# Performance work log

Hardware: AMD Instinct MI355X
Metric: run time of the kernel (lower is better)

The kernel has to match this reference:

```python
import jax, jax.numpy as jnp
import numpy as np

B, H, D = 2048, 50, 400          # batch, history_length, news/category embed dim
S, C = 285, 18                   # num_subcategories, num_categories
NC = 50                          # num_clicks_embed_dim (= history_length table size)
FILL = 1e-30                     # masked_fill value used by the original module


def setup_inputs() -> dict:
    key = jax.random.key(0)
    ks = jax.random.split(key, 9)
    vectors = jax.random.normal(ks[0], (B, H, D), dtype=jnp.float32)
    subcategory = jax.random.randint(ks[1], (B, H), 0, S, dtype=jnp.int32)
    category = jax.random.randint(ks[2], (B, H), 0, C, dtype=jnp.int32)
    subcat_embed = jax.random.normal(ks[3], (S, D), dtype=jnp.float32) * 0.02
    cat_embed = jax.random.normal(ks[4], (C, D), dtype=jnp.float32) * 0.02
    clicks_embed = jax.random.normal(ks[5], (H, NC), dtype=jnp.float32) * 0.02
    w_news = jax.random.normal(ks[6], (D,), dtype=jnp.float32) * 0.05
    w_subcat = jax.random.normal(ks[7], (D + NC,), dtype=jnp.float32) * 0.05
    w_cat = jax.random.normal(ks[8], (D + NC,), dtype=jnp.float32) * 0.05
    return {"vectors": vectors, "subcategory": subcategory, "category": category,
            "subcat_embed": subcat_embed, "cat_embed": cat_embed,
            "clicks_embed": clicks_embed, "w_news": w_news,
            "w_subcat": w_subcat, "w_cat": w_cat}


def reference(vectors, subcategory, category, subcat_embed, cat_embed,
              clicks_embed, w_news, w_subcat, w_cat):
    sub_mask = jax.nn.one_hot(subcategory, S, dtype=vectors.dtype)   # [B,H,S]
    cat_mask = jax.nn.one_hot(category, C, dtype=vectors.dtype)      # [B,H,C]
    sub_to_cat = jnp.einsum('bhs,bhc->bsc', sub_mask, cat_mask)      # [B,S,C]

    # --- news -> subcategory attention pooling ---
    news_scores = jnp.einsum('bhd,d->bh', vectors, w_news)           # [B,H]
    scores = jnp.where(sub_mask > 0, news_scores[:, :, None], FILL)  # [B,H,S]
    news_w = jax.nn.softmax(scores, axis=1)
    sub_news_repr = jnp.einsum('bhs,bhd->bsd', news_w, vectors)      # [B,S,D]
    sub_repr = sub_news_repr + subcat_embed[None]                    # [B,S,D]

    sub_clicks = sub_mask.sum(axis=1)                                # [B,S] float counts
    sub_weights = sub_clicks / sub_clicks.sum(axis=1, keepdims=True)
    sub_clicks_emb = clicks_embed[sub_clicks.astype(jnp.int32)]      # [B,S,NC]

    # --- subcategory -> category attention pooling ---
    sc_scores = jnp.einsum('bsk,k->bs',
                           jnp.concatenate([sub_repr, sub_clicks_emb], axis=2),
                           w_subcat)                                 # [B,S]
    scores2 = jnp.where(sub_to_cat > 0, sc_scores[:, :, None], FILL) # [B,S,C]
    sub_w = jax.nn.softmax(scores2, axis=1)
    cat_sub_repr = jnp.einsum('bsc,bsd->bcd', sub_w, sub_repr)       # [B,C,D]
    cat_repr = cat_sub_repr + cat_embed[None]                        # [B,C,D]

    cat_clicks = cat_mask.sum(axis=1)                                # [B,C]
    cat_weights = cat_clicks / cat_clicks.sum(axis=1, keepdims=True)
    cat_clicks_emb = clicks_embed[cat_clicks.astype(jnp.int32)]      # [B,C,NC]

    # --- category -> user attention pooling (unmasked) ---
    c_scores = jnp.einsum('bck,k->bc',
                          jnp.concatenate([cat_repr, cat_clicks_emb], axis=2),
                          w_cat)                                     # [B,C]
    cat_w = jax.nn.softmax(c_scores, axis=1)
    user_repr = jnp.einsum('bc,bcd->bd', cat_w, cat_repr)            # [B,D]

    return (sub_repr, sub_weights, cat_repr, cat_weights, user_repr)
```

## Files before the change

### kernel.cpp

```cpp
#include <hip/hip_runtime.h>

#define BB 2048
#define HH 50
#define DD 400
#define D4 100
#define SS 285
#define CC 18
#define NCC 50
#define FILLV 1e-30f

static constexpr int BLOCK = 256;

static constexpr size_t OFF1 = (size_t)BB * SS * DD;
static constexpr size_t OFF2 = OFF1 + (size_t)BB * SS;
static constexpr size_t OFF3 = OFF2 + (size_t)BB * CC * DD;
static constexpr size_t OFF4 = OFF3 + (size_t)BB * CC;

#define WS_ETOT 0
#define WS_SCE  400
#define WS_SEW  688
#define WS_CEDS 976
#define WS_CEDC 1026
#define WS_CEW  1076

typedef float f4 __attribute__((ext_vector_type(4)));

__device__ __forceinline__ float dot4(f4 a, f4 b) {
    return a.x * b.x + a.y * b.y + a.z * b.z + a.w * b.w;
}

__global__ void hierec_pre(const float* __restrict__ subcat_embed,
                           const float* __restrict__ cat_embed,
                           const float* __restrict__ clicks_embed,
                           const float* __restrict__ w_subcat,
                           const float* __restrict__ w_cat,
                           float* __restrict__ ws)
{
    const int tid  = threadIdx.x;
    const int lane = tid & 63;
    const int wave = tid >> 6;
    const int wpb  = blockDim.x >> 6;
    const int gw   = blockIdx.x * wpb + wave;
    const int nw   = gridDim.x * wpb;

    for (int s = gw; s < SS; s += nw) {
        float p1 = 0.f, p2 = 0.f;
        for (int d = lane; d < DD; d += 64) {
            float v = subcat_embed[s * DD + d];
            p1 += v * w_subcat[d];
            p2 += v * w_cat[d];
        }
        for (int off = 32; off; off >>= 1) {
            p1 += __shfl_down(p1, off);
            p2 += __shfl_down(p2, off);
        }
        if (lane == 0) { ws[WS_SCE + s] = p1; ws[WS_SEW + s] = p2; }
    }
    if (blockIdx.x == 0) {
        for (int d = tid; d < DD; d += blockDim.x) {
            float a = 0.f;
            for (int s = 0; s < SS; ++s) a += subcat_embed[s * DD + d];
            ws[WS_ETOT + d] = a;
        }
    }
    if (blockIdx.x == 1) {
        for (int k = wave; k < HH; k += wpb) {
            float p1 = 0.f, p2 = 0.f;
            if (lane < NCC) {
                float v = clicks_embed[k * NCC + lane];
                p1 = v * w_subcat[DD + lane];
                p2 = v * w_cat[DD + lane];
            }
            for (int off = 32; off; off >>= 1) {
                p1 += __shfl_down(p1, off);
                p2 += __shfl_down(p2, off);
            }
            if (lane == 0) { ws[WS_CEDS + k] = p1; ws[WS_CEDC + k] = p2; }
        }
    }
    if (blockIdx.x == 2) {
        for (int c = wave; c < CC; c += wpb) {
            float p = 0.f;
            for (int d = lane; d < DD; d += 64) p += cat_embed[c * DD + d] * w_cat[d];
            for (int off = 32; off; off >>= 1) p += __shfl_down(p, off);
            if (lane == 0) ws[WS_CEW + c] = p;
        }
    }
}

__global__ __launch_bounds__(BLOCK, 8) void hierec_main(
    const float* __restrict__ vectors,
    const int*   __restrict__ subcategory,
    const int*   __restrict__ category,
    const float* __restrict__ subcat_embed,
    const float* __restrict__ cat_embed,
    const float* __restrict__ w_news,
    const float* __restrict__ w_subcat,
    const float* __restrict__ w_cat,
    const float* __restrict__ pre,
    float* __restrict__ out)
{
    const int b    = blockIdx.x;
    const int tid  = threadIdx.x;
    const int lane = tid & 63;
    const int wave = tid >> 6;

    __shared__ f4     vt4L[D4];
    __shared__ f4     et4L[D4];
    __shared__ float  coefS[SS];
    __shared__ unsigned long long maskS[SS];
    __shared__ int    cntS[SS];
    __shared__ float  ns1L[HH], ns2L[HH], ns3L[HH];
    __shared__ float  uzL[HH], wNL[HH], scL[HH];
    __shared__ unsigned long long maskL[HH];
    __shared__ int    hsL[HH], hcL[HH], repL[HH], prepL[HH];
    __shared__ float  GmL[CC][HH];
    __shared__ float  mcL[CC], ucL[CC], rZcL[CC], AL[CC], csL[CC], catwL[CC];
    __shared__ int    cntcL[CC];
    __shared__ int    prepCL[HH], prepSL[HH];
    __shared__ float  prepGL[HH];
    __shared__ int    clickedL[HH];
    __shared__ int    unclkL[SS];
    __shared__ int    npL, ndL, nUcnt;
    __shared__ float  PvL, vtwL, etwL;

    const float* vb  = vectors + (size_t)b * HH * DD;
    const f4*    vb4 = (const f4*)vb;
    const f4*    se4 = (const f4*)subcat_embed;
    const f4*    ce4 = (const f4*)cat_embed;

    if (tid < HH) {
        hsL[tid] = subcategory[b * HH + tid];
        hcL[tid] = category[b * HH + tid];
    }
    for (int s = tid; s < SS; s += BLOCK) {
        coefS[s] = 1.f / (float)HH;
        maskS[s] = 0ull;
        cntS[s]  = 0;
    }
    if (tid < D4) {
        et4L[tid] = ((const f4*)pre)[tid];
        f4 z = {0.f, 0.f, 0.f, 0.f};
        vt4L[tid] = z;
    }
    if (tid == 0) nUcnt = 0;
    __syncthreads();

    {
        const f4* wn4 = (const f4*)w_news;
        const f4* ws4 = (const f4*)w_subcat;
        const f4* wc4 = (const f4*)w_cat;
        const bool hi = lane < (D4 - 64);
        f4 vtp0 = {0.f, 0.f, 0.f, 0.f};
        f4 vtp1 = {0.f, 0.f, 0.f, 0.f};
        for (int h = wave; h < HH; h += 4) {
            f4 v0 = __builtin_nontemporal_load(&vb4[h * D4 + lane]);
            float p1 = dot4(v0, wn4[lane]);
            float p2 = dot4(v0, ws4[lane]);
            float p3 = dot4(v0, wc4[lane]);
            vtp0 += v0;
            if (hi) {
                f4 v1 = __builtin_nontemporal_load(&vb4[h * D4 + 64 + lane]);
                p1 += dot4(v1, wn4[64 + lane]);
                p2 += dot4(v1, ws4[64 + lane]);
                p3 += dot4(v1, wc4[64 + lane]);
                vtp1 += v1;
            }
            for (int off = 32; off; off >>= 1) {
                p1 += __shfl_down(p1, off);
                p2 += __shfl_down(p2, off);
                p3 += __shfl_down(p3, off);
            }
            if (lane == 0) { ns1L[h] = p1; ns2L[h] = p2; ns3L[h] = p3; }
        }
        float* vtf = (float*)vt4L;
        atomicAdd(&vtf[4 * lane + 0], vtp0.x);
        atomicAdd(&vtf[4 * lane + 1], vtp0.y);
        atomicAdd(&vtf[4 * lane + 2], vtp0.z);
        atomicAdd(&vtf[4 * lane + 3], vtp0.w);
        if (hi) {
            atomicAdd(&vtf[4 * (64 + lane) + 0], vtp1.x);
            atomicAdd(&vtf[4 * (64 + lane) + 1], vtp1.y);
            atomicAdd(&vtf[4 * (64 + lane) + 2], vtp1.z);
            atomicAdd(&vtf[4 * (64 + lane) + 3], vtp1.w);
        }
    }
    __syncthreads();

    if (tid < HH) {
        const int h = tid;
        const int s = hsL[h], c = hcL[h];
        unsigned long long mask = 0ull, pmask = 0ull;
        for (int j = 0; j < HH; ++j) {
            bool ms = (hsL[j] == s);
            mask  |= (unsigned long long)(ms ? 1 : 0) << j;
            pmask |= (unsigned long long)((ms && hcL[j] == c) ? 1 : 0) << j;
        }
        int cnt = __popcll(mask);
        bool rep = ((__ffsll((long long)mask) - 1) == h);

        float m = FILLV;
        unsigned long long t = mask;
        while (t) { int j = __ffsll((long long)t) - 1; t &= t - 1; m = fmaxf(m, ns1L[j]); }
        float u = expf(FILLV - m);
        float sumE = 0.f, sum2 = 0.f;
        t = mask;
        while (t) {
            int j = __ffsll((long long)t) - 1; t &= t - 1;
            float e = expf(ns1L[j] - m);
            sumE += e;
            sum2 += (e - u) * ns2L[j];
        }
        float Z = sumE + (float)(HH - cnt) * u;
        float vt2 = 0.f;
        for (int j = 0; j < HH; ++j) vt2 += ns2L[j];
        int ci = cnt < (NCC - 1) ? cnt : (NCC - 1);
        float sc = (sum2 + u * vt2) / Z + pre[WS_SCE + s] + pre[WS_CEDS + ci];

        float e_h = expf(ns1L[h] - m);
        float uz = u / Z;
        wNL[h] = (e_h - u) / Z;
        uzL[h] = uz; maskL[h] = mask; scL[h] = sc;
        repL[h]  = rep ? 1 : 0;
        prepL[h] = ((__ffsll((long long)pmask) - 1) == h) ? 1 : 0;
        if (rep) { coefS[s] = uz; maskS[s] = mask; cntS[s] = cnt; }
    } else if (wave == 1) {
        float p = 0.f;
        const float* et = (const float*)et4L;
        for (int d = lane; d < DD; d += 64) p += et[d] * w_cat[d];
        for (int off = 32; off; off >>= 1) p += __shfl_down(p, off);
        if (lane == 0) etwL = p;
    } else if (wave == 2) {
        float p = (lane < HH) ? ns3L[lane] : 0.f;
        for (int off = 32; off; off >>= 1) p += __shfl_down(p, off);
        if (lane == 0) vtwL = p;
    }
    __syncthreads();

    if (tid < CC) {
        const int c = tid;
        float mc = FILLV; int n = 0, cc2 = 0;
        for (int j = 0; j < HH; ++j) {
            if (hcL[j] == c) ++cc2;
            if (prepL[j] && hcL[j] == c) { ++n; mc = fmaxf(mc, scL[j]); }
        }
        float u = expf(FILLV - mc);
        float sumE = 0.f;
        for (int j = 0; j < HH; ++j)
            if (prepL[j] && hcL[j] == c) sumE += expf(scL[j] - mc);
        float Zc = sumE + (float)(SS - n) * u;
        mcL[c] = mc; ucL[c] = u; rZcL[c] = 1.f / Zc; cntcL[c] = cc2;
        __builtin_nontemporal_store((float)cc2 * (1.f / (float)HH),
                                    &out[OFF3 + (size_t)b * CC + c]);
    }
    if (tid == 64) {
        int nd = 0, np = 0;
        float sumUb = 0.f;
        for (int j = 0; j < HH; ++j) {
            if (repL[j]) { clickedL[nd] = hsL[j]; ++nd; sumUb += uzL[j]; }
            if (prepL[j]) { prepCL[np] = hcL[j]; prepSL[np] = hsL[j]; ++np; }
        }
        npL = np; ndL = nd;
        PvL = (float)(SS - nd) * (1.f / (float)HH) + sumUb;
    }
    for (int s = tid; s < SS; s += BLOCK) {
        __builtin_nontemporal_store((float)cntS[s] * (1.f / (float)HH),
                                    &out[OFF1 + (size_t)b * SS + s]);
        if (maskS[s] == 0ull) {
            int p = atomicAdd(&nUcnt, 1);
            unclkL[p] = s;
        }
    }
    __syncthreads();

    for (int idx = tid; idx < CC * HH; idx += BLOCK) {
        int c = idx / HH, h = idx - c * HH;
        bool exists = false;
        unsigned long long t = maskL[h];
        while (t) {
            int k = __ffsll((long long)t) - 1; t &= t - 1;
            if (hcL[k] == c) { exists = true; break; }
        }
        float g = exists ? (expf(scL[h] - mcL[c]) - ucL[c]) : 0.f;
        GmL[c][h] = wNL[h] * (ucL[c] + g);
    }
    if (tid < CC) {
        const int c = tid;
        float A = ucL[c] * PvL;
        for (int j = 0; j < HH; ++j)
            if (prepL[j] && hcL[j] == c)
                A += (expf(scL[j] - mcL[c]) - ucL[c]) * uzL[j];
        AL[c] = A;
    }
    if (tid >= 64 && tid < 64 + HH) {
        int jj = tid - 64;
        if (jj < HH) {
        }
    }
    __syncthreads();
    if (tid < HH && tid < npL) {
        int c = prepCL[tid];
        int s = prepSL[tid];
        float g = 0.f;
        for (int j = 0; j < HH; ++j)
            if (prepL[j] && hcL[j] == c && hsL[j] == s) { g = expf(scL[j] - mcL[c]) - ucL[c]; break; }
        prepGL[tid] = g;
    }
    __syncthreads();

    if (tid < CC) {
        const int c = tid;
        float sG = 0.f;
        for (int h = 0; h < HH; ++h) sG += GmL[c][h] * ns3L[h];
        float sP = 0.f;
        const int np = npL;
        for (int jj = 0; jj < np; ++jj)
            if (prepCL[jj] == c) sP += prepGL[jj] * pre[WS_SEW + prepSL[jj]];
        int ci = cntcL[c] < (NCC - 1) ? cntcL[c] : (NCC - 1);
        csL[c] = rZcL[c] * (AL[c] * vtwL + ucL[c] * etwL + sG + sP)
                 + pre[WS_CEW + c] + pre[WS_CEDC + ci];
    }
    __syncthreads();

    if (tid < CC) {
        float m = csL[0];
        for (int j = 1; j < CC; ++j) m = fmaxf(m, csL[j]);
        float Zc = 0.f;
        for (int j = 0; j < CC; ++j) Zc += expf(csL[j] - m);
        catwL[tid] = expf(csL[tid] - m) / Zc;
    }
    __syncthreads();


    if (tid < D4) {
        const int q = tid;
        const int np = npL;
        f4 uacc = {0.f, 0.f, 0.f, 0.f};
        f4* oc = (f4*)(out + OFF2 + (size_t)b * CC * DD);
        #pragma unroll 1
        for (int c0 = 0; c0 < CC; c0 += 6) {
            f4 vt = vt4L[q], et = et4L[q];
            f4 a[6];
            #pragma unroll
            for (int cc = 0; cc < 6; ++cc) {
                int c = c0 + cc;
                a[cc] = AL[c] * vt + ucL[c] * et;
            }
            for (int h = 0; h < HH; ++h) {
                f4 v = __builtin_nontemporal_load(&vb4[h * D4 + q]);
                #pragma unroll
                for (int cc = 0; cc < 6; ++cc) a[cc] += GmL[c0 + cc][h] * v;
            }
            #pragma unroll
            for (int cc = 0; cc < 6; ++cc) {
                int c = c0 + cc;
                f4 acc = a[cc];
                for (int jj = 0; jj < np; ++jj)
                    if (prepCL[jj] == c) acc += prepGL[jj] * se4[prepSL[jj] * D4 + q];
                acc = rZcL[c] * acc + ce4[c * D4 + q];
                uacc += catwL[c] * acc;
                __builtin_nontemporal_store(acc, &oc[c * D4 + q]);
            }
        }
        f4* ou = (f4*)(out + OFF4 + (size_t)b * DD);
        __builtin_nontemporal_store(uacc, &ou[q]);
    }

    f4* o4 = (f4*)(out + (size_t)b * SS * DD);
    {
        const int tot = ndL * D4;
        for (int i = tid; i < tot; i += BLOCK) {
            int ii = i / D4;
            int q  = i - ii * D4;
            int s  = clickedL[ii];
            f4 acc = coefS[s] * vt4L[q] + se4[s * D4 + q];
            unsigned long long t = maskS[s];
            while (t) {
                int j = __ffsll((long long)t) - 1; t &= t - 1;
                acc += wNL[j] * __builtin_nontemporal_load(&vb4[j * D4 + q]);
            }
            __builtin_nontemporal_store(acc, &o4[s * D4 + q]);
        }
    }

    {
        const int tot = (SS - ndL) * D4;
        const float cst = 1.f / (float)HH;
        for (int i = tid; i < tot; i += BLOCK) {
            int u = i / D4;
            int q = i - u * D4;
            int s = unclkL[u];
            f4 acc = cst * vt4L[q] + se4[s * D4 + q];
            __builtin_nontemporal_store(acc, &o4[s * D4 + q]);
        }
    }
}

extern "C" void kernel_launch(void* const* d_in, const int* in_sizes, int n_in,
                              void* d_out, int out_size, void* d_ws, size_t ws_size,
                              hipStream_t stream) {
    const float* vectors      = (const float*)d_in[0];
    const int*   subcategory  = (const int*)d_in[1];
    const int*   category     = (const int*)d_in[2];
    const float* subcat_embed = (const float*)d_in[3];
    const float* cat_embed    = (const float*)d_in[4];
    const float* clicks_embed = (const float*)d_in[5];
    const float* w_news       = (const float*)d_in[6];
    const float* w_subcat     = (const float*)d_in[7];
    const float* w_cat        = (const float*)d_in[8];
    float* out = (float*)d_out;
    float* ws  = (float*)d_ws;

    hipLaunchKernelGGL(hierec_pre, dim3(32), dim3(256), 0, stream,
                       subcat_embed, cat_embed, clicks_embed, w_subcat, w_cat, ws);
    hipLaunchKernelGGL(hierec_main, dim3(BB), dim3(BLOCK), 0, stream,
                       vectors, subcategory, category, subcat_embed, cat_embed,
                       w_news, w_subcat, w_cat, ws, out);
}
```

Measured before the change: 512.2 us.

## Compute category reprs from already-written subcategory rows instead of re-scanning history

The category stage is reformulated: instead of building an 18x50 Gm matrix and re-streaming all history vectors per category group, it reads back the clicked subcategory rows just written to the output and combines them through per-category segment lists (prepStart), plus a shared total built from a block-wide accumulated weighted sum (Wt4L via LDS atomics). Score terms are likewise derived from per-history weighted sums. Nontemporal loads and stores on the vectors and subcategory outputs become normal accesses so the read-back can hit cache. This cuts redundant global reads and FLOPs but adds an extra barrier, LDS atomics, and a dependence on reading freshly written global memory within the block.

```diff
diff --git a/kernel.cpp b/kernel.cpp
--- a/kernel.cpp
+++ b/kernel.cpp
@@ -24,6 +24,7 @@
 #define WS_CEW  1076
 
 typedef float f4 __attribute__((ext_vector_type(4)));
+typedef unsigned long long u64;
 
 __device__ __forceinline__ float dot4(f4 a, f4 b) {
     return a.x * b.x + a.y * b.y + a.z * b.z + a.w * b.w;
@@ -107,27 +108,29 @@
 
     __shared__ f4     vt4L[D4];
     __shared__ f4     et4L[D4];
+    __shared__ f4     Wt4L[D4];
     __shared__ float  coefS[SS];
-    __shared__ unsigned long long maskS[SS];
+    __shared__ u64    maskS[SS];
     __shared__ int    cntS[SS];
     __shared__ float  ns1L[HH], ns2L[HH], ns3L[HH];
-    __shared__ float  uzL[HH], wNL[HH], scL[HH];
-    __shared__ unsigned long long maskL[HH];
+    __shared__ float  uzL[HH], wNL[HH], scL[HH], Wn3sL[HH];
+    __shared__ u64    maskL[HH];
     __shared__ int    hsL[HH], hcL[HH], repL[HH], prepL[HH];
-    __shared__ float  GmL[CC][HH];
-    __shared__ float  mcL[CC], ucL[CC], rZcL[CC], AL[CC], csL[CC], catwL[CC];
+    __shared__ float  mcL[CC], ucL[CC], rZcL[CC], csL[CC], catwL[CC];
     __shared__ int    cntcL[CC];
-    __shared__ int    prepCL[HH], prepSL[HH];
+    __shared__ int    prepStart[CC + 1];
+    __shared__ int    prepHL[HH], prepSL[HH];
     __shared__ float  prepGL[HH];
     __shared__ int    clickedL[HH];
     __shared__ int    unclkL[SS];
     __shared__ int    npL, ndL, nUcnt;
-    __shared__ float  PvL, vtwL, etwL;
+    __shared__ float  PvL, vtwL, etwL, Wn3totL;
 
     const float* vb  = vectors + (size_t)b * HH * DD;
     const f4*    vb4 = (const f4*)vb;
     const f4*    se4 = (const f4*)subcat_embed;
     const f4*    ce4 = (const f4*)cat_embed;
+    f4* o4 = (f4*)(out + (size_t)b * SS * DD);
 
     if (tid < HH) {
         hsL[tid] = subcategory[b * HH + tid];
@@ -142,6 +145,7 @@
         et4L[tid] = ((const f4*)pre)[tid];
         f4 z = {0.f, 0.f, 0.f, 0.f};
         vt4L[tid] = z;
+        Wt4L[tid] = z;
     }
     if (tid == 0) nUcnt = 0;
     __syncthreads();
@@ -154,13 +158,13 @@
         f4 vtp0 = {0.f, 0.f, 0.f, 0.f};
         f4 vtp1 = {0.f, 0.f, 0.f, 0.f};
         for (int h = wave; h < HH; h += 4) {
-            f4 v0 = __builtin_nontemporal_load(&vb4[h * D4 + lane]);
+            f4 v0 = vb4[h * D4 + lane];
             float p1 = dot4(v0, wn4[lane]);
             float p2 = dot4(v0, ws4[lane]);
             float p3 = dot4(v0, wc4[lane]);
             vtp0 += v0;
             if (hi) {
-                f4 v1 = __builtin_nontemporal_load(&vb4[h * D4 + 64 + lane]);
+                f4 v1 = vb4[h * D4 + 64 + lane];
                 p1 += dot4(v1, wn4[64 + lane]);
                 p2 += dot4(v1, ws4[64 + lane]);
                 p3 += dot4(v1, wc4[64 + lane]);
@@ -190,17 +194,17 @@
     if (tid < HH) {
         const int h = tid;
         const int s = hsL[h], c = hcL[h];
-        unsigned long long mask = 0ull, pmask = 0ull;
+        u64 mask = 0ull, pmask = 0ull;
         for (int j = 0; j < HH; ++j) {
             bool ms = (hsL[j] == s);
-            mask  |= (unsigned long long)(ms ? 1 : 0) << j;
-            pmask |= (unsigned long long)((ms && hcL[j] == c) ? 1 : 0) << j;
+            mask  |= (u64)(ms ? 1 : 0) << j;
+            pmask |= (u64)((ms && hcL[j] == c) ? 1 : 0) << j;
         }
         int cnt = __popcll(mask);
         bool rep = ((__ffsll((long long)mask) - 1) == h);
 
         float m = FILLV;
-        unsigned long long t = mask;
+        u64 t = mask;
         while (t) { int j = __ffsll((long long)t) - 1; t &= t - 1; m = fmaxf(m, ns1L[j]); }
         float u = expf(FILLV - m);
         float sumE = 0.f, sum2 = 0.f;
@@ -252,16 +256,26 @@
         mcL[c] = mc; ucL[c] = u; rZcL[c] = 1.f / Zc; cntcL[c] = cc2;
         __builtin_nontemporal_store((float)cc2 * (1.f / (float)HH),
                                     &out[OFF3 + (size_t)b * CC + c]);
-    }
-    if (tid == 64) {
+    } else if (tid == 64) {
         int nd = 0, np = 0;
         float sumUb = 0.f;
         for (int j = 0; j < HH; ++j) {
             if (repL[j]) { clickedL[nd] = hsL[j]; ++nd; sumUb += uzL[j]; }
-            if (prepL[j]) { prepCL[np] = hcL[j]; prepSL[np] = hsL[j]; ++np; }
+            if (prepL[j]) ++np;
         }
         npL = np; ndL = nd;
         PvL = (float)(SS - nd) * (1.f / (float)HH) + sumUb;
+    } else if (tid >= 128 && tid < 128 + HH) {
+        const int h = tid - 128;
+        float a = 0.f;
+        u64 t = maskL[h];
+        while (t) { int j = __ffsll((long long)t) - 1; t &= t - 1; a += wNL[j] * ns3L[j]; }
+        Wn3sL[h] = a;
+    } else if (wave == 3) {
+        const int l = tid - 192;
+        float p = (l < HH) ? wNL[l] * ns3L[l] : 0.f;
+        for (int off = 32; off; off >>= 1) p += __shfl_down(p, off);
+        if (l == 0) Wn3totL = p;
     }
     for (int s = tid; s < SS; s += BLOCK) {
         __builtin_nontemporal_store((float)cntS[s] * (1.f / (float)HH),
@@ -273,51 +287,25 @@
     }
     __syncthreads();
 
-    for (int idx = tid; idx < CC * HH; idx += BLOCK) {
-        int c = idx / HH, h = idx - c * HH;
-        bool exists = false;
-        unsigned long long t = maskL[h];
-        while (t) {
-            int k = __ffsll((long long)t) - 1; t &= t - 1;
-            if (hcL[k] == c) { exists = true; break; }
-        }
-        float g = exists ? (expf(scL[h] - mcL[c]) - ucL[c]) : 0.f;
-        GmL[c][h] = wNL[h] * (ucL[c] + g);
-    }
     if (tid < CC) {
         const int c = tid;
-        float A = ucL[c] * PvL;
+        int start = 0;
         for (int j = 0; j < HH; ++j)
-            if (prepL[j] && hcL[j] == c)
-                A += (expf(scL[j] - mcL[c]) - ucL[c]) * uzL[j];
-        AL[c] = A;
-    }
-    if (tid >= 64 && tid < 64 + HH) {
-        int jj = tid - 64;
-        if (jj < HH) {
-        }
-    }
-    __syncthreads();
-    if (tid < HH && tid < npL) {
-        int c = prepCL[tid];
-        int s = prepSL[tid];
-        float g = 0.f;
-        for (int j = 0; j < HH; ++j)
-            if (prepL[j] && hcL[j] == c && hsL[j] == s) { g = expf(scL[j] - mcL[c]) - ucL[c]; break; }
-        prepGL[tid] = g;
-    }
-    __syncthreads();
-
-    if (tid < CC) {
-        const int c = tid;
-        float sG = 0.f;
-        for (int h = 0; h < HH; ++h) sG += GmL[c][h] * ns3L[h];
-        float sP = 0.f;
-        const int np = npL;
-        for (int jj = 0; jj < np; ++jj)
-            if (prepCL[jj] == c) sP += prepGL[jj] * pre[WS_SEW + prepSL[jj]];
+            if (prepL[j] && hcL[j] < c) ++start;
+        prepStart[c] = start;
+        if (c == 0) prepStart[CC] = npL;
+        int cur = start;
+        float segs = 0.f;
+        for (int j = 0; j < HH; ++j) {
+            if (prepL[j] && hcL[j] == c) {
+                float g = expf(scL[j] - mcL[c]) - ucL[c];
+                prepHL[cur] = j; prepSL[cur] = hsL[j]; prepGL[cur] = g;
+                segs += g * (uzL[j] * vtwL + Wn3sL[j] + pre[WS_SEW + hsL[j]]);
+                ++cur;
+            }
+        }
         int ci = cntcL[c] < (NCC - 1) ? cntcL[c] : (NCC - 1);
-        csL[c] = rZcL[c] * (AL[c] * vtwL + ucL[c] * etwL + sG + sP)
+        csL[c] = rZcL[c] * (ucL[c] * (PvL * vtwL + etwL + Wn3totL) + segs)
                  + pre[WS_CEW + c] + pre[WS_CEDC + ci];
     }
     __syncthreads();
@@ -331,61 +319,52 @@
     }
     __syncthreads();
 
-
-    if (tid < D4) {
-        const int q = tid;
-        const int np = npL;
-        f4 uacc = {0.f, 0.f, 0.f, 0.f};
-        f4* oc = (f4*)(out + OFF2 + (size_t)b * CC * DD);
-        #pragma unroll 1
-        for (int c0 = 0; c0 < CC; c0 += 6) {
-            f4 vt = vt4L[q], et = et4L[q];
-            f4 a[6];
-            #pragma unroll
-            for (int cc = 0; cc < 6; ++cc) {
-                int c = c0 + cc;
-                a[cc] = AL[c] * vt + ucL[c] * et;
-            }
-            for (int h = 0; h < HH; ++h) {
-                f4 v = __builtin_nontemporal_load(&vb4[h * D4 + q]);
-                #pragma unroll
-                for (int cc = 0; cc < 6; ++cc) a[cc] += GmL[c0 + cc][h] * v;
-            }
-            #pragma unroll
-            for (int cc = 0; cc < 6; ++cc) {
-                int c = c0 + cc;
-                f4 acc = a[cc];
-                for (int jj = 0; jj < np; ++jj)
-                    if (prepCL[jj] == c) acc += prepGL[jj] * se4[prepSL[jj] * D4 + q];
-                acc = rZcL[c] * acc + ce4[c * D4 + q];
-                uacc += catwL[c] * acc;
-                __builtin_nontemporal_store(acc, &oc[c * D4 + q]);
-            }
-        }
-        f4* ou = (f4*)(out + OFF4 + (size_t)b * DD);
-        __builtin_nontemporal_store(uacc, &ou[q]);
-    }
-
-    f4* o4 = (f4*)(out + (size_t)b * SS * DD);
     {
         const int tot = ndL * D4;
         for (int i = tid; i < tot; i += BLOCK) {
             int ii = i / D4;
             int q  = i - ii * D4;
             int s  = clickedL[ii];
-            f4 acc = coefS[s] * vt4L[q] + se4[s * D4 + q];
-            unsigned long long t = maskS[s];
+            f4 wsacc = {0.f, 0.f, 0.f, 0.f};
+            u64 t = maskS[s];
             while (t) {
                 int j = __ffsll((long long)t) - 1; t &= t - 1;
-                acc += wNL[j] * __builtin_nontemporal_load(&vb4[j * D4 + q]);
-            }
-            __builtin_nontemporal_store(acc, &o4[s * D4 + q]);
-        }
+                wsacc += wNL[j] * vb4[j * D4 + q];
+            }
+            float* wt = (float*)&Wt4L[q];
+            atomicAdd(&wt[0], wsacc.x);
+            atomicAdd(&wt[1], wsacc.y);
+            atomicAdd(&wt[2], wsacc.z);
+            atomicAdd(&wt[3], wsacc.w);
+            f4 val = coefS[s] * vt4L[q] + wsacc + se4[s * D4 + q];
+            o4[s * D4 + q] = val;
+        }
+    }
+    __syncthreads();
+
+
+    if (tid < D4) {
+        const int q = tid;
+        f4 SubTot = PvL * vt4L[q] + Wt4L[q] + et4L[q];
+        f4 uacc = {0.f, 0.f, 0.f, 0.f};
+        f4* oc = (f4*)(out + OFF2 + (size_t)b * CC * DD);
+        for (int c = 0; c < CC; ++c) {
+            f4 acc = ucL[c] * SubTot;
+            const int e = prepStart[c + 1];
+            for (int jj = prepStart[c]; jj < e; ++jj)
+                acc += prepGL[jj] * o4[prepSL[jj] * D4 + q];
+            f4 val = rZcL[c] * acc + ce4[c * D4 + q];
+            uacc += catwL[c] * val;
+            __builtin_nontemporal_store(val, &oc[c * D4 + q]);
+        }
+        f4* ou = (f4*)(out + OFF4 + (size_t)b * DD);
+        __builtin_nontemporal_store(uacc, &ou[q]);
     }
 
     {
         const int tot = (SS - ndL) * D4;
         const float cst = 1.f / (float)HH;
+        #pragma unroll 4
         for (int i = tid; i < tot; i += BLOCK) {
             int u = i / D4;
             int q = i - u * D4;
```

New measurement: 511.9 us. About the same (-0.0%).
